# Kernel tuning notes

Hardware: AMD Instinct MI355X
Metric: run time of the kernel (lower is better)

## Reference

```python
import jax, jax.numpy as jnp
import numpy as np

DT = 0.01  # integration timestep of the Euler-discretized plant


def setup_inputs() -> dict:
    key = jax.random.key(0)
    ks = jax.random.split(key, 8)
    B, T, n, m, c = 2048, 128, 16, 8, 4
    state0 = jax.random.normal(ks[0], (B, n), dtype=jnp.float32)
    controls = jax.random.normal(ks[1], (B, T, c), dtype=jnp.float32)
    obs = jax.random.normal(ks[2], (B, T, m), dtype=jnp.float32)
    A = jax.random.normal(ks[3], (n, n), dtype=jnp.float32) * 0.3
    Bc = jax.random.normal(ks[4], (n, c), dtype=jnp.float32)
    H = jax.random.normal(ks[5], (m, n), dtype=jnp.float32) * 0.5
    Mq = jax.random.normal(ks[6], (n, n), dtype=jnp.float32)
    Q = (Mq @ Mq.T) * (0.01 / n) + 0.01 * jnp.eye(n, dtype=jnp.float32)  # SPD process noise
    Mr = jax.random.normal(ks[7], (m, m), dtype=jnp.float32)
    R = (Mr @ Mr.T) * (0.1 / m) + 0.1 * jnp.eye(m, dtype=jnp.float32)    # SPD obs noise
    P0 = jnp.broadcast_to(jnp.eye(n, dtype=jnp.float32), (B, n, n))       # initial covariance
    return {"state0": state0, "P0": P0, "controls": controls, "obs": obs,
            "A": A, "Bc": Bc, "H": H, "Q": Q, "R": R}


def reference(state0, P0, controls, obs, A, Bc, H, Q, R):
    # Batched Kalman filter (predict + update) over T steps, then RTS smoothing.
    B, n = state0.shape
    T = controls.shape[1]
    I = jnp.eye(n, dtype=state0.dtype)
    F = I + DT * A  # constant Jacobian of the linear Euler plant

    def plant(s, u):  # s: [B,n], u: [B,c]
        return s + DT * (s @ A.T + u @ Bc.T)

    def filt_step(carry, xs):
        s_f, P_f = carry          # filtered state/cov from previous step
        u, y = xs                 # [B,c], [B,m]
        # --- prediction: state_ = plant(s), P_ = F P F^T + Q ---
        s_p = plant(s_f, u)
        P_p = jnp.einsum('ij,bjk,lk->bil', F, P_f, F) + Q
        # --- filtering: K = P H^T (H P H^T + R)^{-1} ---
        PHt = jnp.einsum('bij,kj->bik', P_p, H)       # [B,n,m]
        S = jnp.einsum('ki,bim->bkm', H, PHt) + R      # [B,m,m]
        K = PHt @ jnp.linalg.inv(S)                    # [B,n,m]
        innov = y - s_p @ H.T                          # obs - obs_pred
        s_new = s_p + jnp.einsum('bnm,bm->bn', K, innov)
        P_new = P_p - jnp.einsum('bnm,mj,bjk->bnk', K, H, P_p)
        return (s_new, P_new), (s_p, P_p, s_new, P_new)

    xs = (jnp.swapaxes(controls, 0, 1), jnp.swapaxes(obs, 0, 1))  # [T,B,...]
    _, (s_p_seq, P_p_seq, s_f_seq, P_f_seq) = jax.lax.scan(filt_step, (state0, P0), xs)

    # --- RTS smoothing: A = P_f F^T P_p^{-1}; backward recursion ---
    def smooth_step(carry, xs):
        s_s_next, P_s_next = carry
        s_f, P_f, s_p_next, P_p_next = xs
        Pinv = jnp.linalg.inv(P_p_next)
        G = jnp.einsum('bij,kj,bkl->bil', P_f, F, Pinv)   # smoothing gain [B,n,n]
        s_s = s_f + jnp.einsum('bnm,bm->bn', G, s_s_next - s_p_next)
        P_s = P_f + G @ (P_s_next - P_p_next) @ jnp.swapaxes(G, -1, -2)
        return (s_s, P_s), s_s

    xs_s = (s_f_seq[:-1], P_f_seq[:-1], s_p_seq[1:], P_p_seq[1:])
    init = (s_f_seq[-1], P_f_seq[-1])
    _, s_s_seq = jax.lax.scan(smooth_step, init, xs_s, reverse=True)
    s_s_all = jnp.concatenate([s_s_seq, s_f_seq[-1:]], axis=0)  # [T,B,n]
    return jnp.swapaxes(s_s_all, 0, 1)  # smoothed states [B,T,n]
```

## Files before the change

kernel.cpp:

```cpp
#include <hip/hip_runtime.h>

#define NB 2048
#define TS 128
#define NS 16
#define MS 8
#define CS 4
#define DTC 0.01f

#define K_OFF 0
#define K_SZ (TS*NS*MS)
#define G_OFF (K_OFF + K_SZ)
#define G_SZ ((TS-1)*NS*NS)
#define PP_OFF (G_OFF + G_SZ)
#define PP_SZ (TS*NS*NS)
#define PF_OFF (PP_OFF + PP_SZ)
#define PF_SZ (TS*NS*NS)
#define A_OFF (PF_OFF + PF_SZ)
#define A_SZ (TS*NS*NS)
#define M_OFF (A_OFF + A_SZ)
#define M_SZ (TS*NS*CS)

#define GSHFL(v, k) __shfl((v), ((tid & 48) | (k)), 64)

#define LBAR() do { \
    asm volatile("s_waitcnt lgkmcnt(0)" ::: "memory"); \
    __builtin_amdgcn_s_barrier(); \
    asm volatile("" ::: "memory"); \
} while (0)

__global__ __launch_bounds__(256) void cov_kernel(
    const float* __restrict__ Ag, const float* __restrict__ Hg,
    const float* __restrict__ Qg, const float* __restrict__ Rg,
    const float* __restrict__ P0g, const float* __restrict__ Bcg,
    float* __restrict__ Kw, float* __restrict__ Ppw, float* __restrict__ Pfw,
    float* __restrict__ Aw, float* __restrict__ Mw)
{
    __shared__ float Fs[NS][NS], Qs[NS][NS];
    __shared__ float Hs[MS][NS], HFs[MS][NS], QHt[NS][MS];
    __shared__ float Rs[MS][MS], Rbar[MS][MS], HBcs[MS][CS], Bcs[NS][CS];
    __shared__ float Pf[NS][NS], Pp[NS][NS], TP[NS][NS], Ws[MS][NS];
    __shared__ float PHt[NS][MS], HP[MS][NS], Ks[NS][MS];
    __shared__ float Sg[MS][MS];

    const int tid = threadIdx.x;
    const int i = tid >> 4, j = tid & 15;

    float Fri[NS];
#pragma unroll
    for (int k = 0; k < NS; ++k) Fri[k] = ((i == k) ? 1.f : 0.f) + DTC * Ag[i*NS + k];

    Fs[i][j] = ((i == j) ? 1.f : 0.f) + DTC * Ag[tid];
    Qs[i][j] = Qg[tid];
    if (tid < MS*NS) Hs[tid >> 4][tid & 15] = Hg[tid];
    if (tid < MS*MS) Rs[tid >> 3][tid & 7] = Rg[tid];
    if (tid < NS*CS) Bcs[tid >> 2][tid & 3] = Bcg[tid];
    Pf[i][j] = P0g[tid];
    LBAR();

    if (tid < MS*NS) {
        const int a = tid >> 4, k = tid & 15;
        float acc = 0.f;
#pragma unroll
        for (int m = 0; m < NS; ++m) acc += Hs[a][m] * Fs[m][k];
        HFs[a][k] = acc;
    } else {
        const int e = tid - 128, ii = e >> 3, b = e & 7;
        float acc = 0.f;
#pragma unroll
        for (int k = 0; k < NS; ++k) acc += Qs[ii][k] * Hs[b][k];
        QHt[ii][b] = acc;
    }
    if (tid < MS*CS) {
        const int r = tid >> 2, c = tid & 3;
        float acc = 0.f;
#pragma unroll
        for (int k = 0; k < NS; ++k) acc += Hs[r][k] * Bcs[k][c];
        HBcs[r][c] = acc;
    }
    LBAR();

    if (tid < MS*MS) {
        const int r = tid >> 3, c = tid & 7;
        float acc = Rs[r][c];
#pragma unroll
        for (int k = 0; k < NS; ++k) acc += Hs[r][k] * QHt[k][c];
        Rbar[r][c] = acc;
    }
    LBAR();

    for (int t = 0; t < TS; ++t) {
        {
            float a0 = 0.f, a1 = 0.f;
#pragma unroll
            for (int k = 0; k < NS; k += 2) { a0 += Fri[k]*Pf[k][j]; a1 += Fri[k+1]*Pf[k+1][j]; }
            TP[i][j] = a0 + a1;
            if (tid < MS*NS) {
                const int a = tid >> 4, jj = tid & 15;
                float w0 = 0.f, w1 = 0.f;
#pragma unroll
                for (int k = 0; k < NS; k += 2) { w0 += HFs[a][k]*Pf[k][jj]; w1 += HFs[a][k+1]*Pf[k+1][jj]; }
                Ws[a][jj] = w0 + w1;
            }
        }
        LBAR();

        {
            float c0 = Qs[i][j], c1 = 0.f;
#pragma unroll
            for (int k = 0; k < NS; k += 2) { c0 += TP[i][k]*Fs[j][k]; c1 += TP[i][k+1]*Fs[j][k+1]; }
            const float ppv = c0 + c1;
            Pp[i][j] = ppv;
            Ppw[t*(NS*NS) + tid] = ppv;
            if (tid < NS*MS) {
                const int ii = tid >> 3, l = tid & 7;
                float b0 = QHt[ii][l], b1 = 0.f;
#pragma unroll
                for (int k = 0; k < NS; k += 2) { b0 += TP[ii][k]*HFs[l][k]; b1 += TP[ii][k+1]*HFs[l][k+1]; }
                PHt[ii][l] = b0 + b1;
            } else if (tid < 192) {
                const int e = tid - 128, r = e >> 3, c = e & 7;
                float s0 = Rbar[r][c], s1 = 0.f;
#pragma unroll
                for (int k = 0; k < NS; k += 2) { s0 += Ws[r][k]*HFs[c][k]; s1 += Ws[r][k+1]*HFs[c][k+1]; }
                Sg[r][c] = s0 + s1;
            }
        }
        LBAR();

        if (tid < 128) {
            const int ii = tid >> 3, m = tid & 7;
            float Sr[MS][MS];
#pragma unroll
            for (int a = 0; a < MS; ++a) {
                const float4 x0 = *(const float4*)&Sg[a][0];
                const float4 x1 = *(const float4*)&Sg[a][4];
                Sr[a][0]=x0.x; Sr[a][1]=x0.y; Sr[a][2]=x0.z; Sr[a][3]=x0.w;
                Sr[a][4]=x1.x; Sr[a][5]=x1.y; Sr[a][6]=x1.z; Sr[a][7]=x1.w;
            }
            float rds[MS];
#pragma unroll
            for (int p = 0; p < MS; ++p) {
                const float rd = 1.f / Sr[p][p]; rds[p] = rd;
#pragma unroll
                for (int r = p+1; r < MS; ++r) {
                    const float f = Sr[r][p] * rd; Sr[r][p] = f;
#pragma unroll
                    for (int c = p+1; c < MS; ++c) Sr[r][c] -= f * Sr[p][c];
                }
            }
            float yv[MS];
#pragma unroll
            for (int r = 0; r < MS; ++r) {
                float v = (r == m) ? 1.f : 0.f;
#pragma unroll
                for (int c = 0; c < r; ++c) v -= Sr[r][c] * yv[c];
                yv[r] = v;
            }
            float xv[MS];
#pragma unroll
            for (int r = MS-1; r >= 0; --r) {
                float v = yv[r];
#pragma unroll
                for (int c = r+1; c < MS; ++c) v -= Sr[r][c] * xv[c];
                xv[r] = v * rds[r];
            }
            const float4 p0 = *(const float4*)&PHt[ii][0];
            const float4 p1 = *(const float4*)&PHt[ii][4];
            float kv = p0.x*xv[0] + p0.y*xv[1] + p0.z*xv[2] + p0.w*xv[3]
                     + p1.x*xv[4] + p1.y*xv[5] + p1.z*xv[6] + p1.w*xv[7];
            Ks[ii][m] = kv;
            Kw[t*(NS*MS) + tid] = kv;
        } else {
            const int e = tid - 128, m = e >> 4, jj = e & 15;
            float v = 0.f;
#pragma unroll
            for (int k = 0; k < NS; ++k) v += Hs[m][k] * Pp[k][jj];
            HP[m][jj] = v;
        }
        LBAR();

        {
            float kr[MS];
            *(float4*)&kr[0] = *(const float4*)&Ks[i][0];
            *(float4*)&kr[4] = *(const float4*)&Ks[i][4];
            float pf = Pp[i][j], av = Fs[i][j];
#pragma unroll
            for (int m = 0; m < MS; ++m) { pf -= kr[m] * HP[m][j]; av -= kr[m] * HFs[m][j]; }
            Pf[i][j] = pf;
            Pfw[t*(NS*NS) + tid] = pf;
            Aw[t*(NS*NS) + tid] = av;
            if (tid < NS*CS) {
                const int ri = tid >> 2, c = tid & 3;
                float mv = Bcs[ri][c];
#pragma unroll
                for (int m = 0; m < MS; ++m) mv -= Ks[ri][m] * HBcs[m][c];
                Mw[t*(NS*CS) + tid] = DTC * mv;
            }
        }
        LBAR();
    }
}

__global__ __launch_bounds__(256) void gprep_kernel(
    const float* __restrict__ Ag,
    const float* __restrict__ Ppw, const float* __restrict__ Pfw,
    float* __restrict__ Gw,
    const float* __restrict__ ctrl, const float* __restrict__ obsg,
    const float* __restrict__ Kw, const float* __restrict__ Mw,
    float* __restrict__ outp)
{
    const int tid = threadIdx.x;
    __shared__ float aug0[NS][NS], aug1[NS][NS], Pfs[NS][NS], Wsh[NS][NS];

    if (blockIdx.x < TS-1) {
        const int t = blockIdx.x;
        const int r = tid >> 4, cl = tid & 15;

        float Frc[NS];
#pragma unroll
        for (int k = 0; k < NS; ++k) Frc[k] = ((cl == k) ? 1.f : 0.f) + DTC * Ag[cl*NS + k];

        aug0[r][cl] = Ppw[(t+1)*(NS*NS) + tid];
        aug1[r][cl] = (r == cl) ? 1.f : 0.f;
        Pfs[r][cl]  = Pfw[t*(NS*NS) + tid];
        __syncthreads();

        for (int p = 0; p < NS; ++p) {
            const float a0 = aug0[r][cl], a1 = aug1[r][cl];
            const float d  = aug0[p][p];
            const float pa = aug0[p][cl], pb = aug1[p][cl];
            const float f  = aug0[r][p];
            __syncthreads();
            const float rd = 1.f / d;
            if (r == p) { aug0[r][cl] = pa * rd;       aug1[r][cl] = pb * rd; }
            else        { const float frd = f * rd;
                          aug0[r][cl] = a0 - frd * pa; aug1[r][cl] = a1 - frd * pb; }
            __syncthreads();
        }

        float w0 = 0.f, w1 = 0.f;
#pragma unroll
        for (int k = 0; k < NS; k += 2) { w0 += Pfs[r][k]*Frc[k]; w1 += Pfs[r][k+1]*Frc[k+1]; }
        Wsh[r][cl] = w0 + w1;
        __syncthreads();

        float g0 = 0.f, g1 = 0.f;
#pragma unroll
        for (int k = 0; k < NS; k += 2) { g0 += Wsh[r][k]*aug1[k][cl]; g1 += Wsh[r][k+1]*aug1[k+1][cl]; }
        Gw[t*(NS*NS) + tid] = g0 + g1;
    } else {
        const int g = (blockIdx.x - (TS-1)) * 256 + tid;
        const int b = g >> 11;
        const int rem = g & 2047;
        const int t = rem >> 4, i = rem & 15;

        const float4 u  = *(const float4*)(ctrl + (size_t)b*TS*CS + t*CS);
        const float4 y0 = *(const float4*)(obsg + (size_t)b*TS*MS + t*MS);
        const float4 y1 = *(const float4*)(obsg + (size_t)b*TS*MS + t*MS + 4);
        const float4 mr = *(const float4*)(Mw + t*(NS*CS) + i*CS);
        const float4 k0 = *(const float4*)(Kw + t*(NS*MS) + i*MS);
        const float4 k1 = *(const float4*)(Kw + t*(NS*MS) + i*MS + 4);

        float v = mr.x*u.x + mr.y*u.y + mr.z*u.z + mr.w*u.w;
        v += k0.x*y0.x + k0.y*y0.y + k0.z*y0.z + k0.w*y0.w;
        v += k1.x*y1.x + k1.y*y1.y + k1.z*y1.z + k1.w*y1.w;
        outp[g] = v;
    }
}

#define FWD_LOAD(B, T) do { \
    const float* ap_ = Aw + (T)*(NS*NS) + lane*NS; \
    B##a0 = *(const float4*)(ap_);      B##a1 = *(const float4*)(ap_ + 4); \
    B##a2 = *(const float4*)(ap_ + 8);  B##a3 = *(const float4*)(ap_ + 12); \
    B##bt = myslot[(T)*128]; \
} while (0)

#define FWD_STEP(T, B, TL) do { \
    float p0_ = B##bt, p1_ = 0.f, p2_ = 0.f, p3_ = 0.f; \
    p0_ += B##a0.x*GSHFL(s,0)  + B##a0.y*GSHFL(s,1); \
    p1_ += B##a0.z*GSHFL(s,2)  + B##a0.w*GSHFL(s,3); \
    p2_ += B##a1.x*GSHFL(s,4)  + B##a1.y*GSHFL(s,5); \
    p3_ += B##a1.z*GSHFL(s,6)  + B##a1.w*GSHFL(s,7); \
    p0_ += B##a2.x*GSHFL(s,8)  + B##a2.y*GSHFL(s,9); \
    p1_ += B##a2.z*GSHFL(s,10) + B##a2.w*GSHFL(s,11); \
    p2_ += B##a3.x*GSHFL(s,12) + B##a3.y*GSHFL(s,13); \
    p3_ += B##a3.z*GSHFL(s,14) + B##a3.w*GSHFL(s,15); \
    const float sn_ = (p0_ + p1_) + (p2_ + p3_); \
    myslot[(T)*128] = sn_; \
    s = sn_; \
    if ((TL) < TS) FWD_LOAD(B, TL); \
} while (0)

#define BWD_LOAD(B, T) do { \
    const float* gp_ = Gw + (T)*(NS*NS) + lane*NS; \
    B##g0 = *(const float4*)(gp_);      B##g1 = *(const float4*)(gp_ + 4); \
    B##g2 = *(const float4*)(gp_ + 8);  B##g3 = *(const float4*)(gp_ + 12); \
    B##u  = *(const float4*)(up + ((T)+1)*CS); \
    B##sf = myslot[(T)*128]; \
} while (0)

#define BWD_STEP(T, B, TL) do { \
    float p0_ = Bci[0]*B##u.x + Bci[1]*B##u.y; \
    float p1_ = Bci[2]*B##u.z + Bci[3]*B##u.w; \
    float p2_ = 0.f, p3_ = 0.f; \
    _Pragma("unroll") \
    for (int k = 0; k < NS; k += 4) { \
        p0_ += Fi[k  ] * GSHFL(B##sf, k); \
        p1_ += Fi[k+1] * GSHFL(B##sf, k+1); \
        p2_ += Fi[k+2] * GSHFL(B##sf, k+2); \
        p3_ += Fi[k+3] * GSHFL(B##sf, k+3); \
    } \
    const float diff_ = ss - ((p0_ + p1_) + (p2_ + p3_)); \
    float a0_ = B##g0.x*GSHFL(diff_,0)  + B##g0.y*GSHFL(diff_,1); \
    a0_      += B##g0.z*GSHFL(diff_,2)  + B##g0.w*GSHFL(diff_,3); \
    float a1_ = B##g1.x*GSHFL(diff_,4)  + B##g1.y*GSHFL(diff_,5); \
    a1_      += B##g1.z*GSHFL(diff_,6)  + B##g1.w*GSHFL(diff_,7); \
    float a2_ = B##g2.x*GSHFL(diff_,8)  + B##g2.y*GSHFL(diff_,9); \
    a2_      += B##g2.z*GSHFL(diff_,10) + B##g2.w*GSHFL(diff_,11); \
    float a3_ = B##g3.x*GSHFL(diff_,12) + B##g3.y*GSHFL(diff_,13); \
    a3_      += B##g3.z*GSHFL(diff_,14) + B##g3.w*GSHFL(diff_,15); \
    const float sn_ = B##sf + ((a0_ + a1_) + (a2_ + a3_)); \
    ob[(T)*NS + lane] = sn_; \
    ss = sn_; \
    if ((TL) >= 0) BWD_LOAD(B, TL); \
} while (0)

__global__ __launch_bounds__(128, 1) void fb_kernel(
    const float* __restrict__ s0g, const float* __restrict__ Aw,
    const float* __restrict__ Gw, const float* __restrict__ ctrl,
    const float* __restrict__ Ag, const float* __restrict__ Bcg,
    float* __restrict__ outp)
{
    extern __shared__ float sfs[];
    const int tid  = threadIdx.x;
    const int lane = tid & 15;
    const int wb   = tid >> 4;
    const int b    = blockIdx.x * 8 + wb;
    float* ob = outp + (size_t)b * TS * NS;
    float* myslot = sfs + wb*NS + lane;

    {
        const float4* src = (const float4*)(outp + (size_t)(blockIdx.x*8) * TS * NS);
        float4* dst = (float4*)sfs;
        for (int idx = tid; idx < 4096; idx += 128) {
            const int wb2 = idx >> 9;
            const int k   = idx & 511;
            const float4 v = src[idx];
            dst[(k >> 2)*32 + wb2*4 + (k & 3)] = v;
        }
    }
    __syncthreads();

    {
        float s = s0g[b*NS + lane];
        float4 Aa0, Aa1, Aa2, Aa3; float Abt;
        float4 Ba0, Ba1, Ba2, Ba3; float Bbt;
        float4 Ca0, Ca1, Ca2, Ca3; float Cbt;
        float4 Da0, Da1, Da2, Da3; float Dbt;
        FWD_LOAD(A, 0); FWD_LOAD(B, 1); FWD_LOAD(C, 2); FWD_LOAD(D, 3);

        for (int tb = 0; tb <= TS-4; tb += 4) {
            FWD_STEP(tb,   A, tb+4);
            FWD_STEP(tb+1, B, tb+5);
            FWD_STEP(tb+2, C, tb+6);
            FWD_STEP(tb+3, D, tb+7);
        }
    }

    {
        float Fi[NS], Bci[CS];
#pragma unroll
        for (int k = 0; k < NS; ++k) Fi[k] = ((lane == k) ? 1.f : 0.f) + DTC * Ag[lane*NS + k];
#pragma unroll
        for (int k = 0; k < CS; ++k) Bci[k] = DTC * Bcg[lane*CS + k];
        const float* up = ctrl + (size_t)b * TS * CS;

        float ss = myslot[(TS-1)*128];
        ob[(TS-1)*NS + lane] = ss;

        float4 Ag0, Ag1, Ag2, Ag3, Au; float Asf;
        float4 Bg0, Bg1, Bg2, Bg3, Bu; float Bsf;
        float4 Cg0, Cg1, Cg2, Cg3, Cu; float Csf;
        float4 Dg0, Dg1, Dg2, Dg3, Du; float Dsf;
        BWD_LOAD(A, TS-2); BWD_LOAD(B, TS-3); BWD_LOAD(C, TS-4); BWD_LOAD(D, TS-5);

        for (int tb = TS-2; tb >= 6; tb -= 4) {
            BWD_STEP(tb,   A, tb-4);
            BWD_STEP(tb-1, B, tb-5);
            BWD_STEP(tb-2, C, tb-6);
            BWD_STEP(tb-3, D, tb-7);
        }
        BWD_STEP(2, A, -1);
        BWD_STEP(1, B, -1);
        BWD_STEP(0, C, -1);
    }
}

extern "C" void kernel_launch(void* const* d_in, const int* in_sizes, int n_in,
                              void* d_out, int out_size, void* d_ws, size_t ws_size,
                              hipStream_t stream)
{
    (void)out_size; (void)ws_size;

    const float *s0 = nullptr, *P0 = nullptr, *ctrl = nullptr, *obs = nullptr;
    const float *A = nullptr, *Bc = nullptr, *H = nullptr, *Q = nullptr, *R = nullptr;
    for (int idx = 0; idx < n_in; ++idx) {
        const float* p = (const float*)d_in[idx];
        switch (in_sizes[idx]) {
            case NB*NS:        s0   = p; break;
            case NB*NS*NS:     P0   = p; break;
            case NB*TS*CS:     ctrl = p; break;
            case NB*TS*MS:     obs  = p; break;
            case MS*NS:        H    = p; break;
            case NS*NS:        if (!A)  A  = p; else Q = p; break;
            case MS*MS:        if (!Bc) Bc = p; else R = p; break;
            default: break;
        }
    }

    float* ws  = (float*)d_ws;
    float* Kw  = ws + K_OFF;
    float* Gw  = ws + G_OFF;
    float* Ppw = ws + PP_OFF;
    float* Pfw = ws + PF_OFF;
    float* Aw  = ws + A_OFF;
    float* Mw  = ws + M_OFF;
    float* out = (float*)d_out;

    hipLaunchKernelGGL(cov_kernel, dim3(1), dim3(256), 0, stream,
                       A, H, Q, R, P0, Bc, Kw, Ppw, Pfw, Aw, Mw);
    hipLaunchKernelGGL(gprep_kernel, dim3((TS-1) + NB*TS*NS/256), dim3(256), 0, stream,
                       A, Ppw, Pfw, Gw, ctrl, obs, Kw, Mw, out);
    hipLaunchKernelGGL(fb_kernel, dim3(NB/8), dim3(128), TS*8*NS*sizeof(float), stream,
                       s0, Aw, Gw, ctrl, A, Bc, out);
}
```

Before: 312.7 us.

## Precompute (I - G F) and G Bc so smoothing drops off-critical-path work

New measurement: 324.1 us. +3.6%, slower.

```diff
diff --git a/kernel.cpp b/kernel.cpp
--- a/kernel.cpp
+++ b/kernel.cpp
@@ -19,6 +19,10 @@
 #define A_SZ (TS*NS*NS)
 #define M_OFF (A_OFF + A_SZ)
 #define M_SZ (TS*NS*CS)
+#define E_OFF (M_OFF + M_SZ)
+#define E_SZ (TS*NS*NS)
+#define N_OFF (E_OFF + E_SZ)
+#define N_SZ (TS*NS*CS)
 
 #define GSHFL(v, k) __shfl((v), ((tid & 48) | (k)), 64)
 
@@ -202,52 +206,71 @@
 }
 
 __global__ __launch_bounds__(256) void gprep_kernel(
-    const float* __restrict__ Ag,
+    const float* __restrict__ Ag, const float* __restrict__ Bcg,
     const float* __restrict__ Ppw, const float* __restrict__ Pfw,
-    float* __restrict__ Gw,
+    float* __restrict__ Gw, float* __restrict__ Ew, float* __restrict__ Nw,
     const float* __restrict__ ctrl, const float* __restrict__ obsg,
     const float* __restrict__ Kw, const float* __restrict__ Mw,
     float* __restrict__ outp)
 {
     const int tid = threadIdx.x;
-    __shared__ float aug0[NS][NS], aug1[NS][NS], Pfs[NS][NS], Wsh[NS][NS];
+    __shared__ float aug[2][NS][2*NS];
+    __shared__ float Pfs[NS][NS], Wsh[NS][NS], Fsh[NS][NS], Gsh[NS][NS];
+    __shared__ float Bcs[NS][CS];
 
     if (blockIdx.x < TS-1) {
         const int t = blockIdx.x;
-        const int r = tid >> 4, cl = tid & 15;
+        const int r = tid >> 4, c0 = tid & 15;
 
         float Frc[NS];
 #pragma unroll
-        for (int k = 0; k < NS; ++k) Frc[k] = ((cl == k) ? 1.f : 0.f) + DTC * Ag[cl*NS + k];
-
-        aug0[r][cl] = Ppw[(t+1)*(NS*NS) + tid];
-        aug1[r][cl] = (r == cl) ? 1.f : 0.f;
-        Pfs[r][cl]  = Pfw[t*(NS*NS) + tid];
+        for (int k = 0; k < NS; ++k) Frc[k] = ((c0 == k) ? 1.f : 0.f) + DTC * Ag[c0*NS + k];
+
+        Fsh[r][c0] = ((r == c0) ? 1.f : 0.f) + DTC * Ag[tid];
+        Pfs[r][c0] = Pfw[t*(NS*NS) + tid];
+        aug[0][r][c0]      = Ppw[(t+1)*(NS*NS) + tid];
+        aug[0][r][c0 + NS] = (r == c0) ? 1.f : 0.f;
+        if (tid < NS*CS) Bcs[tid >> 2][tid & 3] = Bcg[tid];
         __syncthreads();
 
         for (int p = 0; p < NS; ++p) {
-            const float a0 = aug0[r][cl], a1 = aug1[r][cl];
-            const float d  = aug0[p][p];
-            const float pa = aug0[p][cl], pb = aug1[p][cl];
-            const float f  = aug0[r][p];
+            const int cur = p & 1, nxt = cur ^ 1;
+            const float rd = 1.f / aug[cur][p][p];
+            const float arp = aug[cur][r][p];
+#pragma unroll
+            for (int half = 0; half < 2; ++half) {
+                const int c = c0 + half*NS;
+                const float pivc = aug[cur][p][c];
+                const float arc  = aug[cur][r][c];
+                aug[nxt][r][c] = (r == p) ? pivc * rd : arc - (arp * rd) * pivc;
+            }
             __syncthreads();
-            const float rd = 1.f / d;
-            if (r == p) { aug0[r][cl] = pa * rd;       aug1[r][cl] = pb * rd; }
-            else        { const float frd = f * rd;
-                          aug0[r][cl] = a0 - frd * pa; aug1[r][cl] = a1 - frd * pb; }
-            __syncthreads();
         }
 
         float w0 = 0.f, w1 = 0.f;
 #pragma unroll
         for (int k = 0; k < NS; k += 2) { w0 += Pfs[r][k]*Frc[k]; w1 += Pfs[r][k+1]*Frc[k+1]; }
-        Wsh[r][cl] = w0 + w1;
+        Wsh[r][c0] = w0 + w1;
         __syncthreads();
 
         float g0 = 0.f, g1 = 0.f;
 #pragma unroll
-        for (int k = 0; k < NS; k += 2) { g0 += Wsh[r][k]*aug1[k][cl]; g1 += Wsh[r][k+1]*aug1[k+1][cl]; }
-        Gw[t*(NS*NS) + tid] = g0 + g1;
+        for (int k = 0; k < NS; k += 2) { g0 += Wsh[r][k]*aug[0][k][NS+c0]; g1 += Wsh[r][k+1]*aug[0][k+1][NS+c0]; }
+        const float gv = g0 + g1;
+        Gw[t*(NS*NS) + tid] = gv;
+        Gsh[r][c0] = gv;
+        __syncthreads();
+
+        float e0 = 0.f, e1 = 0.f;
+#pragma unroll
+        for (int k = 0; k < NS; k += 2) { e0 += Gsh[r][k]*Fsh[k][c0]; e1 += Gsh[r][k+1]*Fsh[k+1][c0]; }
+        Ew[t*(NS*NS) + tid] = ((r == c0) ? 1.f : 0.f) - (e0 + e1);
+        if (c0 < CS) {
+            float nv = 0.f;
+#pragma unroll
+            for (int k = 0; k < NS; ++k) nv += Gsh[r][k]*Bcs[k][c0];
+            Nw[t*(NS*CS) + r*CS + c0] = DTC * nv;
+        }
     } else {
         const int g = (blockIdx.x - (TS-1)) * 256 + tid;
         const int b = g >> 11;
@@ -295,31 +318,34 @@
     const float* gp_ = Gw + (T)*(NS*NS) + lane*NS; \
     B##g0 = *(const float4*)(gp_);      B##g1 = *(const float4*)(gp_ + 4); \
     B##g2 = *(const float4*)(gp_ + 8);  B##g3 = *(const float4*)(gp_ + 12); \
-    B##u  = *(const float4*)(up + ((T)+1)*CS); \
-    B##sf = myslot[(T)*128]; \
+    const float* ep_ = Ew + (T)*(NS*NS) + lane*NS; \
+    const float4 e0_ = *(const float4*)(ep_);      const float4 e1_ = *(const float4*)(ep_ + 4); \
+    const float4 e2_ = *(const float4*)(ep_ + 8);  const float4 e3_ = *(const float4*)(ep_ + 12); \
+    const float4 n_  = *(const float4*)(Nw + (T)*(NS*CS) + lane*CS); \
+    const float4 u_  = *(const float4*)(up + ((T)+1)*CS); \
+    const float sf_  = myslot[(T)*128]; \
+    float v0_ = e0_.x*GSHFL(sf_,0)  + e0_.y*GSHFL(sf_,1); \
+    v0_      += e0_.z*GSHFL(sf_,2)  + e0_.w*GSHFL(sf_,3); \
+    float v1_ = e1_.x*GSHFL(sf_,4)  + e1_.y*GSHFL(sf_,5); \
+    v1_      += e1_.z*GSHFL(sf_,6)  + e1_.w*GSHFL(sf_,7); \
+    float v2_ = e2_.x*GSHFL(sf_,8)  + e2_.y*GSHFL(sf_,9); \
+    v2_      += e2_.z*GSHFL(sf_,10) + e2_.w*GSHFL(sf_,11); \
+    float v3_ = e3_.x*GSHFL(sf_,12) + e3_.y*GSHFL(sf_,13); \
+    v3_      += e3_.z*GSHFL(sf_,14) + e3_.w*GSHFL(sf_,15); \
+    const float nu_ = n_.x*u_.x + n_.y*u_.y + n_.z*u_.z + n_.w*u_.w; \
+    B##v = ((v0_ + v1_) + (v2_ + v3_)) - nu_; \
 } while (0)
 
 #define BWD_STEP(T, B, TL) do { \
-    float p0_ = Bci[0]*B##u.x + Bci[1]*B##u.y; \
-    float p1_ = Bci[2]*B##u.z + Bci[3]*B##u.w; \
-    float p2_ = 0.f, p3_ = 0.f; \
-    _Pragma("unroll") \
-    for (int k = 0; k < NS; k += 4) { \
-        p0_ += Fi[k  ] * GSHFL(B##sf, k); \
-        p1_ += Fi[k+1] * GSHFL(B##sf, k+1); \
-        p2_ += Fi[k+2] * GSHFL(B##sf, k+2); \
-        p3_ += Fi[k+3] * GSHFL(B##sf, k+3); \
-    } \
-    const float diff_ = ss - ((p0_ + p1_) + (p2_ + p3_)); \
-    float a0_ = B##g0.x*GSHFL(diff_,0)  + B##g0.y*GSHFL(diff_,1); \
-    a0_      += B##g0.z*GSHFL(diff_,2)  + B##g0.w*GSHFL(diff_,3); \
-    float a1_ = B##g1.x*GSHFL(diff_,4)  + B##g1.y*GSHFL(diff_,5); \
-    a1_      += B##g1.z*GSHFL(diff_,6)  + B##g1.w*GSHFL(diff_,7); \
-    float a2_ = B##g2.x*GSHFL(diff_,8)  + B##g2.y*GSHFL(diff_,9); \
-    a2_      += B##g2.z*GSHFL(diff_,10) + B##g2.w*GSHFL(diff_,11); \
-    float a3_ = B##g3.x*GSHFL(diff_,12) + B##g3.y*GSHFL(diff_,13); \
-    a3_      += B##g3.z*GSHFL(diff_,14) + B##g3.w*GSHFL(diff_,15); \
-    const float sn_ = B##sf + ((a0_ + a1_) + (a2_ + a3_)); \
+    float a0_ = B##g0.x*GSHFL(ss,0)  + B##g0.y*GSHFL(ss,1); \
+    a0_      += B##g0.z*GSHFL(ss,2)  + B##g0.w*GSHFL(ss,3); \
+    float a1_ = B##g1.x*GSHFL(ss,4)  + B##g1.y*GSHFL(ss,5); \
+    a1_      += B##g1.z*GSHFL(ss,6)  + B##g1.w*GSHFL(ss,7); \
+    float a2_ = B##g2.x*GSHFL(ss,8)  + B##g2.y*GSHFL(ss,9); \
+    a2_      += B##g2.z*GSHFL(ss,10) + B##g2.w*GSHFL(ss,11); \
+    float a3_ = B##g3.x*GSHFL(ss,12) + B##g3.y*GSHFL(ss,13); \
+    a3_      += B##g3.z*GSHFL(ss,14) + B##g3.w*GSHFL(ss,15); \
+    const float sn_ = B##v + ((a0_ + a1_) + (a2_ + a3_)); \
     ob[(T)*NS + lane] = sn_; \
     ss = sn_; \
     if ((TL) >= 0) BWD_LOAD(B, TL); \
@@ -327,8 +353,8 @@
 
 __global__ __launch_bounds__(128, 1) void fb_kernel(
     const float* __restrict__ s0g, const float* __restrict__ Aw,
-    const float* __restrict__ Gw, const float* __restrict__ ctrl,
-    const float* __restrict__ Ag, const float* __restrict__ Bcg,
+    const float* __restrict__ Gw, const float* __restrict__ Ew,
+    const float* __restrict__ Nw, const float* __restrict__ ctrl,
     float* __restrict__ outp)
 {
     extern __shared__ float sfs[];
@@ -368,20 +394,15 @@
     }
 
     {
-        float Fi[NS], Bci[CS];
-#pragma unroll
-        for (int k = 0; k < NS; ++k) Fi[k] = ((lane == k) ? 1.f : 0.f) + DTC * Ag[lane*NS + k];
-#pragma unroll
-        for (int k = 0; k < CS; ++k) Bci[k] = DTC * Bcg[lane*CS + k];
         const float* up = ctrl + (size_t)b * TS * CS;
 
         float ss = myslot[(TS-1)*128];
         ob[(TS-1)*NS + lane] = ss;
 
-        float4 Ag0, Ag1, Ag2, Ag3, Au; float Asf;
-        float4 Bg0, Bg1, Bg2, Bg3, Bu; float Bsf;
-        float4 Cg0, Cg1, Cg2, Cg3, Cu; float Csf;
-        float4 Dg0, Dg1, Dg2, Dg3, Du; float Dsf;
+        float4 Ag0, Ag1, Ag2, Ag3; float Av;
+        float4 Bg0, Bg1, Bg2, Bg3; float Bv;
+        float4 Cg0, Cg1, Cg2, Cg3; float Cv;
+        float4 Dg0, Dg1, Dg2, Dg3; float Dv;
         BWD_LOAD(A, TS-2); BWD_LOAD(B, TS-3); BWD_LOAD(C, TS-4); BWD_LOAD(D, TS-5);
 
         for (int tb = TS-2; tb >= 6; tb -= 4) {
@@ -425,12 +446,14 @@
     float* Pfw = ws + PF_OFF;
     float* Aw  = ws + A_OFF;
     float* Mw  = ws + M_OFF;
+    float* Ew  = ws + E_OFF;
+    float* Nw  = ws + N_OFF;
     float* out = (float*)d_out;
 
     hipLaunchKernelGGL(cov_kernel, dim3(1), dim3(256), 0, stream,
                        A, H, Q, R, P0, Bc, Kw, Ppw, Pfw, Aw, Mw);
     hipLaunchKernelGGL(gprep_kernel, dim3((TS-1) + NB*TS*NS/256), dim3(256), 0, stream,
-                       A, Ppw, Pfw, Gw, ctrl, obs, Kw, Mw, out);
+                       A, Bc, Ppw, Pfw, Gw, Ew, Nw, ctrl, obs, Kw, Mw, out);
     hipLaunchKernelGGL(fb_kernel, dim3(NB/8), dim3(128), TS*8*NS*sizeof(float), stream,
-                       s0, Aw, Gw, ctrl, A, Bc, out);
+                       s0, Aw, Gw, Ew, Nw, ctrl, out);
 }
```

## Run covariance recursion in a single wavefront to drop block barriers

Applied to the files above, without the earlier changes.

Result: slower. 388.3 us (+24.2%).

```diff
diff --git a/kernel.cpp b/kernel.cpp
--- a/kernel.cpp
+++ b/kernel.cpp
@@ -22,120 +22,163 @@
 
 #define GSHFL(v, k) __shfl((v), ((tid & 48) | (k)), 64)
 
-#define LBAR() do { \
-    asm volatile("s_waitcnt lgkmcnt(0)" ::: "memory"); \
-    __builtin_amdgcn_s_barrier(); \
-    asm volatile("" ::: "memory"); \
-} while (0)
-
-__global__ __launch_bounds__(256) void cov_kernel(
+#define WFENCE() asm volatile("s_waitcnt lgkmcnt(0)" ::: "memory")
+
+__global__ __launch_bounds__(64) void cov_wave(
     const float* __restrict__ Ag, const float* __restrict__ Hg,
     const float* __restrict__ Qg, const float* __restrict__ Rg,
     const float* __restrict__ P0g, const float* __restrict__ Bcg,
     float* __restrict__ Kw, float* __restrict__ Ppw, float* __restrict__ Pfw,
     float* __restrict__ Aw, float* __restrict__ Mw)
 {
-    __shared__ float Fs[NS][NS], Qs[NS][NS];
-    __shared__ float Hs[MS][NS], HFs[MS][NS], QHt[NS][MS];
-    __shared__ float Rs[MS][MS], Rbar[MS][MS], HBcs[MS][CS], Bcs[NS][CS];
-    __shared__ float Pf[NS][NS], Pp[NS][NS], TP[NS][NS], Ws[MS][NS];
-    __shared__ float PHt[NS][MS], HP[MS][NS], Ks[NS][MS];
-    __shared__ float Sg[MS][MS];
-
-    const int tid = threadIdx.x;
-    const int i = tid >> 4, j = tid & 15;
-
-    float Fri[NS];
-#pragma unroll
-    for (int k = 0; k < NS; ++k) Fri[k] = ((i == k) ? 1.f : 0.f) + DTC * Ag[i*NS + k];
-
-    Fs[i][j] = ((i == j) ? 1.f : 0.f) + DTC * Ag[tid];
-    Qs[i][j] = Qg[tid];
-    if (tid < MS*NS) Hs[tid >> 4][tid & 15] = Hg[tid];
-    if (tid < MS*MS) Rs[tid >> 3][tid & 7] = Rg[tid];
-    if (tid < NS*CS) Bcs[tid >> 2][tid & 3] = Bcg[tid];
-    Pf[i][j] = P0g[tid];
-    LBAR();
-
-    if (tid < MS*NS) {
-        const int a = tid >> 4, k = tid & 15;
-        float acc = 0.f;
-#pragma unroll
-        for (int m = 0; m < NS; ++m) acc += Hs[a][m] * Fs[m][k];
-        HFs[a][k] = acc;
-    } else {
-        const int e = tid - 128, ii = e >> 3, b = e & 7;
-        float acc = 0.f;
-#pragma unroll
-        for (int k = 0; k < NS; ++k) acc += Qs[ii][k] * Hs[b][k];
-        QHt[ii][b] = acc;
-    }
-    if (tid < MS*CS) {
-        const int r = tid >> 2, c = tid & 3;
+    __shared__ float Fs[NS][NS], Qs[NS][NS], Hs[MS][NS];
+    __shared__ float HFs[MS][NS], QHt[NS][MS], Rs[MS][MS], Rbar[MS][MS];
+    __shared__ float Bcs[NS][CS], HBcs[MS][CS];
+    __shared__ float Pf[NS][NS], TP[NS][NS], Ws[MS][NS];
+    __shared__ float PHt[NS][MS], HP[MS][NS], Sg[MS][MS], Ks[NS][MS];
+
+    const int L  = threadIdx.x;
+    const int i  = L >> 2, q = L & 3, jb = q * 4;
+    const int a8 = L >> 3, c8 = L & 7;
+    const int jw = (L & 7) * 2;
+
+#pragma unroll
+    for (int s = 0; s < 4; ++s) {
+        const int tid = L + s*64, ii = tid >> 4, jj = tid & 15;
+        Fs[ii][jj] = ((ii == jj) ? 1.f : 0.f) + DTC * Ag[tid];
+        Qs[ii][jj] = Qg[tid];
+        Pf[ii][jj] = P0g[tid];
+    }
+#pragma unroll
+    for (int s = 0; s < 2; ++s) {
+        const int e = L + s*64;
+        Hs[e >> 4][e & 15] = Hg[e];
+    }
+    Rs[a8][c8] = Rg[L];
+    Bcs[i][q]  = Bcg[L];
+    WFENCE();
+
+#pragma unroll
+    for (int s = 0; s < 2; ++s) {
+        const int e = L + s*64;
+        { const int a = e >> 4, k = e & 15;
+          float acc = 0.f;
+#pragma unroll
+          for (int m = 0; m < NS; ++m) acc += Hs[a][m] * Fs[m][k];
+          HFs[a][k] = acc; }
+        { const int ii = e >> 3, b = e & 7;
+          float acc = 0.f;
+#pragma unroll
+          for (int k = 0; k < NS; ++k) acc += Qs[ii][k] * Hs[b][k];
+          QHt[ii][b] = acc; }
+    }
+    if (L < MS*CS) {
+        const int r = L >> 2, c = L & 3;
         float acc = 0.f;
 #pragma unroll
         for (int k = 0; k < NS; ++k) acc += Hs[r][k] * Bcs[k][c];
         HBcs[r][c] = acc;
     }
-    LBAR();
-
-    if (tid < MS*MS) {
-        const int r = tid >> 3, c = tid & 7;
-        float acc = Rs[r][c];
-#pragma unroll
-        for (int k = 0; k < NS; ++k) acc += Hs[r][k] * QHt[k][c];
-        Rbar[r][c] = acc;
-    }
-    LBAR();
+    WFENCE();
+
+    {
+        float acc = Rs[a8][c8];
+#pragma unroll
+        for (int k = 0; k < NS; ++k) acc += Hs[a8][k] * QHt[k][c8];
+        Rbar[a8][c8] = acc;
+    }
+    WFENCE();
+
+    float Fri[NS], HFa[NS], F4[4][NS], HF2[2][NS];
+#pragma unroll
+    for (int k = 0; k < NS; ++k) Fri[k] = Fs[i][k];
+#pragma unroll
+    for (int k = 0; k < NS; ++k) HFa[k] = HFs[a8][k];
+#pragma unroll
+    for (int c = 0; c < 4; ++c)
+#pragma unroll
+        for (int k = 0; k < NS; ++k) F4[c][k] = Fs[jb + c][k];
+#pragma unroll
+    for (int d = 0; d < 2; ++d)
+#pragma unroll
+        for (int k = 0; k < NS; ++k) HF2[d][k] = HFs[2*q + d][k];
+    WFENCE();
 
     for (int t = 0; t < TS; ++t) {
+        float t0 = 0.f, t1 = 0.f, t2 = 0.f, t3 = 0.f;
+#pragma unroll
+        for (int k = 0; k < NS; ++k) {
+            const float4 pk = *(const float4*)&Pf[k][jb];
+            t0 += Fri[k]*pk.x; t1 += Fri[k]*pk.y; t2 += Fri[k]*pk.z; t3 += Fri[k]*pk.w;
+        }
+        float w0 = 0.f, w1 = 0.f;
+#pragma unroll
+        for (int k = 0; k < NS; ++k) {
+            const float2 p2 = *(const float2*)&Pf[k][jw];
+            w0 += HFa[k]*p2.x; w1 += HFa[k]*p2.y;
+        }
+        *(float4*)&TP[i][jb] = make_float4(t0, t1, t2, t3);
+        *(float2*)&Ws[a8][jw] = make_float2(w0, w1);
+        WFENCE();
+
+        float tpr[NS];
+#pragma unroll
+        for (int k4 = 0; k4 < 4; ++k4) {
+            const float4 v = *(const float4*)&TP[i][k4*4];
+            tpr[k4*4] = v.x; tpr[k4*4+1] = v.y; tpr[k4*4+2] = v.z; tpr[k4*4+3] = v.w;
+        }
+        float pp[4];
         {
-            float a0 = 0.f, a1 = 0.f;
-#pragma unroll
-            for (int k = 0; k < NS; k += 2) { a0 += Fri[k]*Pf[k][j]; a1 += Fri[k+1]*Pf[k+1][j]; }
-            TP[i][j] = a0 + a1;
-            if (tid < MS*NS) {
-                const int a = tid >> 4, jj = tid & 15;
-                float w0 = 0.f, w1 = 0.f;
-#pragma unroll
-                for (int k = 0; k < NS; k += 2) { w0 += HFs[a][k]*Pf[k][jj]; w1 += HFs[a][k+1]*Pf[k+1][jj]; }
-                Ws[a][jj] = w0 + w1;
-            }
-        }
-        LBAR();
-
+            const float4 qv = *(const float4*)&Qs[i][jb];
+            pp[0] = qv.x; pp[1] = qv.y; pp[2] = qv.z; pp[3] = qv.w;
+#pragma unroll
+            for (int c = 0; c < 4; ++c) {
+                float acc = pp[c];
+#pragma unroll
+                for (int k = 0; k < NS; ++k) acc += tpr[k]*F4[c][k];
+                pp[c] = acc;
+            }
+        }
+        float ph0, ph1;
         {
-            float c0 = Qs[i][j], c1 = 0.f;
-#pragma unroll
-            for (int k = 0; k < NS; k += 2) { c0 += TP[i][k]*Fs[j][k]; c1 += TP[i][k+1]*Fs[j][k+1]; }
-            const float ppv = c0 + c1;
-            Pp[i][j] = ppv;
-            Ppw[t*(NS*NS) + tid] = ppv;
-            if (tid < NS*MS) {
-                const int ii = tid >> 3, l = tid & 7;
-                float b0 = QHt[ii][l], b1 = 0.f;
-#pragma unroll
-                for (int k = 0; k < NS; k += 2) { b0 += TP[ii][k]*HFs[l][k]; b1 += TP[ii][k+1]*HFs[l][k+1]; }
-                PHt[ii][l] = b0 + b1;
-            } else if (tid < 192) {
-                const int e = tid - 128, r = e >> 3, c = e & 7;
-                float s0 = Rbar[r][c], s1 = 0.f;
-#pragma unroll
-                for (int k = 0; k < NS; k += 2) { s0 += Ws[r][k]*HFs[c][k]; s1 += Ws[r][k+1]*HFs[c][k+1]; }
-                Sg[r][c] = s0 + s1;
-            }
-        }
-        LBAR();
-
-        if (tid < 128) {
-            const int ii = tid >> 3, m = tid & 7;
+            const float2 qh = *(const float2*)&QHt[i][2*q];
+            ph0 = qh.x; ph1 = qh.y;
+#pragma unroll
+            for (int k = 0; k < NS; ++k) { ph0 += tpr[k]*HF2[0][k]; ph1 += tpr[k]*HF2[1][k]; }
+        }
+        float wr[NS];
+#pragma unroll
+        for (int k4 = 0; k4 < 4; ++k4) {
+            const float4 v = *(const float4*)&Ws[a8][k4*4];
+            wr[k4*4] = v.x; wr[k4*4+1] = v.y; wr[k4*4+2] = v.z; wr[k4*4+3] = v.w;
+        }
+        float sv = Rbar[a8][c8];
+#pragma unroll
+        for (int k4 = 0; k4 < 4; ++k4) {
+            const float4 h = *(const float4*)&HFs[c8][k4*4];
+            sv += wr[k4*4]*h.x + wr[k4*4+1]*h.y + wr[k4*4+2]*h.z + wr[k4*4+3]*h.w;
+        }
+        float hp0 = QHt[jw][a8], hp1 = QHt[jw+1][a8];
+#pragma unroll
+        for (int k4 = 0; k4 < 4; ++k4) {
+            const float4 f0 = *(const float4*)&Fs[jw][k4*4];
+            const float4 f1 = *(const float4*)&Fs[jw+1][k4*4];
+            hp0 += wr[k4*4]*f0.x + wr[k4*4+1]*f0.y + wr[k4*4+2]*f0.z + wr[k4*4+3]*f0.w;
+            hp1 += wr[k4*4]*f1.x + wr[k4*4+1]*f1.y + wr[k4*4+2]*f1.z + wr[k4*4+3]*f1.w;
+        }
+        *(float2*)&PHt[i][2*q] = make_float2(ph0, ph1);
+        Sg[a8][c8] = sv;
+        *(float2*)&HP[a8][jw] = make_float2(hp0, hp1);
+        WFENCE();
+
+        {
             float Sr[MS][MS];
 #pragma unroll
-            for (int a = 0; a < MS; ++a) {
-                const float4 x0 = *(const float4*)&Sg[a][0];
-                const float4 x1 = *(const float4*)&Sg[a][4];
-                Sr[a][0]=x0.x; Sr[a][1]=x0.y; Sr[a][2]=x0.z; Sr[a][3]=x0.w;
-                Sr[a][4]=x1.x; Sr[a][5]=x1.y; Sr[a][6]=x1.z; Sr[a][7]=x1.w;
+            for (int rr = 0; rr < MS; ++rr) {
+                const float4 x0 = *(const float4*)&Sg[rr][0];
+                const float4 x1 = *(const float4*)&Sg[rr][4];
+                Sr[rr][0]=x0.x; Sr[rr][1]=x0.y; Sr[rr][2]=x0.z; Sr[rr][3]=x0.w;
+                Sr[rr][4]=x1.x; Sr[rr][5]=x1.y; Sr[rr][6]=x1.z; Sr[rr][7]=x1.w;
             }
             float rds[MS];
 #pragma unroll
@@ -148,6 +191,7 @@
                     for (int c = p+1; c < MS; ++c) Sr[r][c] -= f * Sr[p][c];
                 }
             }
+            const int m = c8;
             float yv[MS];
 #pragma unroll
             for (int r = 0; r < MS; ++r) {
@@ -164,40 +208,48 @@
                 for (int c = r+1; c < MS; ++c) v -= Sr[r][c] * xv[c];
                 xv[r] = v * rds[r];
             }
-            const float4 p0 = *(const float4*)&PHt[ii][0];
-            const float4 p1 = *(const float4*)&PHt[ii][4];
-            float kv = p0.x*xv[0] + p0.y*xv[1] + p0.z*xv[2] + p0.w*xv[3]
-                     + p1.x*xv[4] + p1.y*xv[5] + p1.z*xv[6] + p1.w*xv[7];
-            Ks[ii][m] = kv;
-            Kw[t*(NS*MS) + tid] = kv;
-        } else {
-            const int e = tid - 128, m = e >> 4, jj = e & 15;
-            float v = 0.f;
-#pragma unroll
-            for (int k = 0; k < NS; ++k) v += Hs[m][k] * Pp[k][jj];
-            HP[m][jj] = v;
-        }
-        LBAR();
+            const float4 pA0 = *(const float4*)&PHt[a8][0];
+            const float4 pA1 = *(const float4*)&PHt[a8][4];
+            const float4 pB0 = *(const float4*)&PHt[a8+8][0];
+            const float4 pB1 = *(const float4*)&PHt[a8+8][4];
+            const float kv0 = pA0.x*xv[0] + pA0.y*xv[1] + pA0.z*xv[2] + pA0.w*xv[3]
+                            + pA1.x*xv[4] + pA1.y*xv[5] + pA1.z*xv[6] + pA1.w*xv[7];
+            const float kv1 = pB0.x*xv[0] + pB0.y*xv[1] + pB0.z*xv[2] + pB0.w*xv[3]
+                            + pB1.x*xv[4] + pB1.y*xv[5] + pB1.z*xv[6] + pB1.w*xv[7];
+            Ks[a8][m]     = kv0;
+            Ks[a8 + 8][m] = kv1;
+            Kw[t*(NS*MS) + L]      = kv0;
+            Kw[t*(NS*MS) + 64 + L] = kv1;
+        }
+        WFENCE();
 
         {
             float kr[MS];
-            *(float4*)&kr[0] = *(const float4*)&Ks[i][0];
-            *(float4*)&kr[4] = *(const float4*)&Ks[i][4];
-            float pf = Pp[i][j], av = Fs[i][j];
-#pragma unroll
-            for (int m = 0; m < MS; ++m) { pf -= kr[m] * HP[m][j]; av -= kr[m] * HFs[m][j]; }
-            Pf[i][j] = pf;
-            Pfw[t*(NS*NS) + tid] = pf;
-            Aw[t*(NS*NS) + tid] = av;
-            if (tid < NS*CS) {
-                const int ri = tid >> 2, c = tid & 3;
-                float mv = Bcs[ri][c];
-#pragma unroll
-                for (int m = 0; m < MS; ++m) mv -= Ks[ri][m] * HBcs[m][c];
-                Mw[t*(NS*CS) + tid] = DTC * mv;
-            }
-        }
-        LBAR();
+            const float4 k0 = *(const float4*)&Ks[i][0];
+            const float4 k1 = *(const float4*)&Ks[i][4];
+            kr[0]=k0.x; kr[1]=k0.y; kr[2]=k0.z; kr[3]=k0.w;
+            kr[4]=k1.x; kr[5]=k1.y; kr[6]=k1.z; kr[7]=k1.w;
+            float pfv[4] = {pp[0], pp[1], pp[2], pp[3]};
+            float av [4] = {Fri[jb], Fri[jb+1], Fri[jb+2], Fri[jb+3]};
+#pragma unroll
+            for (int m2 = 0; m2 < MS; ++m2) {
+                const float4 hpv = *(const float4*)&HP[m2][jb];
+                const float4 hfv = *(const float4*)&HFs[m2][jb];
+                pfv[0] -= kr[m2]*hpv.x; pfv[1] -= kr[m2]*hpv.y;
+                pfv[2] -= kr[m2]*hpv.z; pfv[3] -= kr[m2]*hpv.w;
+                av[0]  -= kr[m2]*hfv.x; av[1]  -= kr[m2]*hfv.y;
+                av[2]  -= kr[m2]*hfv.z; av[3]  -= kr[m2]*hfv.w;
+            }
+            *(float4*)&Pf[i][jb] = make_float4(pfv[0], pfv[1], pfv[2], pfv[3]);
+            *(float4*)&Ppw[t*(NS*NS) + i*NS + jb] = make_float4(pp[0], pp[1], pp[2], pp[3]);
+            *(float4*)&Pfw[t*(NS*NS) + i*NS + jb] = make_float4(pfv[0], pfv[1], pfv[2], pfv[3]);
+            *(float4*)&Aw [t*(NS*NS) + i*NS + jb] = make_float4(av[0], av[1], av[2], av[3]);
+            float mv = Bcs[i][q];
+#pragma unroll
+            for (int m2 = 0; m2 < MS; ++m2) mv -= kr[m2] * HBcs[m2][q];
+            Mw[t*(NS*CS) + L] = DTC * mv;
+        }
+        WFENCE();
     }
 }
 
@@ -427,7 +479,7 @@
     float* Mw  = ws + M_OFF;
     float* out = (float*)d_out;
 
-    hipLaunchKernelGGL(cov_kernel, dim3(1), dim3(256), 0, stream,
+    hipLaunchKernelGGL(cov_wave, dim3(1), dim3(64), 0, stream,
                        A, H, Q, R, P0, Bc, Kw, Ppw, Pfw, Aw, Mw);
     hipLaunchKernelGGL(gprep_kernel, dim3((TS-1) + NB*TS*NS/256), dim3(256), 0, stream,
                        A, Ppw, Pfw, Gw, ctrl, obs, Kw, Mw, out);
```
